# Performance work log

Measured on AMD Instinct MI355X. Metric: run time of the kernel, lower is better.

The kernel has to match this reference:

```python
import jax, jax.numpy as jnp
import numpy as np

DROPOUT_P = 0.0  # undefined global `dropout_p` in source; pinned to 0 (identity) for determinism


def setup_inputs() -> dict:
    key = jax.random.key(0)
    k1, k2, k3 = jax.random.split(key, 3)
    B, Lq, Lk, D = 16, 4096, 4096, 64
    return {
        "query": jax.random.normal(k1, (B, Lq, D), dtype=jnp.float32),
        "key": jax.random.normal(k2, (B, Lk, D), dtype=jnp.float32),
        "value": jax.random.normal(k3, (B, Lk, D), dtype=jnp.float32),
        "scale_factor": jnp.ones((1,), dtype=jnp.float32),
    }


def reference(query, key, value, scale_factor):
    # scores: [B, Lq, Lk] -- the large HBM-materialized intermediate
    scores = jnp.einsum("bqd,bkd->bqk", query, key) / scale_factor
    probs = jax.nn.softmax(scores, axis=-1)
    # dropout with p = DROPOUT_P = 0.0 is the identity
    out = jnp.einsum("bqk,bkd->bqd", probs, value)
    return out
```

## Files before the change

### kernel.cpp

```cpp
#include <hip/hip_runtime.h>
#include <hip/hip_fp16.h>

typedef _Float16 half2_t __attribute__((ext_vector_type(2)));
typedef _Float16 half4_t __attribute__((ext_vector_type(4)));
typedef _Float16 half8_t __attribute__((ext_vector_type(8)));
typedef float   float4_t __attribute__((ext_vector_type(4)));

static __device__ __forceinline__ half2_t cvt_pk(float a, float b) {
    return __builtin_bit_cast(half2_t, __builtin_amdgcn_cvt_pkrtz(a, b));
}
static __device__ __forceinline__ half4_t cvt_pk4(float a, float b, float c, float d) {
    half2_t lo = cvt_pk(a, b), hi = cvt_pk(c, d);
    half4_t r;
    r[0] = lo[0]; r[1] = lo[1]; r[2] = hi[0]; r[3] = hi[1];
    return r;
}

namespace {
constexpr int kB      = 16;
constexpr int kL      = 4096;
constexpr int kD      = 64;
constexpr int kQTile  = 128;
constexpr int kBK     = 64;
constexpr int kStride = 72;
}

__global__ __launch_bounds__(256, 2)
void fa_fwd(const float* __restrict__ Q, const float* __restrict__ K,
            const float* __restrict__ V, const float* __restrict__ scale_ptr,
            float* __restrict__ Out)
{
    __shared__ __align__(16) _Float16 Ksh[kBK * kStride];
    __shared__ __align__(16) _Float16 Vsh[kD * kStride];

    const int tid  = threadIdx.x;
    const int wave = tid >> 6;
    const int lane = tid & 63;
    const int c    = lane & 15;
    const int qd   = lane >> 4;

    const int b  = blockIdx.y;
    const int q0 = blockIdx.x * kQTile + wave * 32;

    const float qscale = 1.4426950408889634f / scale_ptr[0];

    const float* Qb = Q + (size_t)b * kL * kD;
    const float* Kb = K + (size_t)b * kL * kD;
    const float* Vb = V + (size_t)b * kL * kD;

    half8_t qfrag[2][2];
#pragma unroll
    for (int qt = 0; qt < 2; ++qt) {
        const float* qrow = Qb + (size_t)(q0 + qt * 16 + c) * kD;
#pragma unroll
        for (int dk = 0; dk < 2; ++dk) {
            const float* p = qrow + dk * 32 + qd * 8;
            half8_t h;
#pragma unroll
            for (int j = 0; j < 8; ++j) h[j] = (_Float16)(p[j] * qscale);
            qfrag[qt][dk] = h;
        }
    }

    float4_t O[2][4];
#pragma unroll
    for (int qt = 0; qt < 2; ++qt)
#pragma unroll
        for (int dt = 0; dt < 4; ++dt) O[qt][dt] = (float4_t)0.0f;

    float m_run[2] = {-__builtin_inff(), -__builtin_inff()};
    float lpart[2] = {0.0f, 0.0f};

    float4 pk[4], pv[4];
#pragma unroll
    for (int i = 0; i < 4; ++i) {
        const int tk = tid + 256 * i;
        pk[i] = *(const float4*)(Kb + (size_t)(tk >> 4) * kD + (tk & 15) * 4);
        pv[i] = *(const float4*)(Vb + (size_t)(tk & 63) * kD + (tk >> 6) * 4);
    }

    for (int kb = 0; kb < kL; kb += kBK) {
        __syncthreads();

#pragma unroll
        for (int i = 0; i < 4; ++i) {
            const int tk = tid + 256 * i;
            *(half4_t*)(&Ksh[(tk >> 4) * kStride + (tk & 15) * 4]) =
                cvt_pk4(pk[i].x, pk[i].y, pk[i].z, pk[i].w);
        }
#pragma unroll
        for (int i = 0; i < 4; ++i) {
            const int tk  = tid + 256 * i;
            const int row = tk & 63;
            const int c4  = tk >> 6;
            Vsh[(c4 * 4 + 0) * kStride + row] = (_Float16)pv[i].x;
            Vsh[(c4 * 4 + 1) * kStride + row] = (_Float16)pv[i].y;
            Vsh[(c4 * 4 + 2) * kStride + row] = (_Float16)pv[i].z;
            Vsh[(c4 * 4 + 3) * kStride + row] = (_Float16)pv[i].w;
        }
        __syncthreads();

        {
            const int nb = (kb + kBK) & (kL - 1);
            const float* Kn = Kb + (size_t)nb * kD;
            const float* Vn = Vb + (size_t)nb * kD;
#pragma unroll
            for (int i = 0; i < 4; ++i) {
                const int tk = tid + 256 * i;
                pk[i] = *(const float4*)(Kn + (size_t)(tk >> 4) * kD + (tk & 15) * 4);
                pv[i] = *(const float4*)(Vn + (size_t)(tk & 63) * kD + (tk >> 6) * 4);
            }
        }

        half8_t kf[4][2];
#pragma unroll
        for (int kt = 0; kt < 4; ++kt)
#pragma unroll
            for (int dk = 0; dk < 2; ++dk)
                kf[kt][dk] = *(const half8_t*)(&Ksh[(kt * 16 + c) * kStride + dk * 32 + qd * 8]);

        float4_t S[4][2];
#pragma unroll
        for (int kt = 0; kt < 4; ++kt)
#pragma unroll
            for (int qt = 0; qt < 2; ++qt) {
                float4_t acc = {-32.0f, -32.0f, -32.0f, -32.0f};
                acc = __builtin_amdgcn_mfma_f32_16x16x32_f16(kf[kt][0], qfrag[qt][0], acc, 0, 0, 0);
                acc = __builtin_amdgcn_mfma_f32_16x16x32_f16(kf[kt][1], qfrag[qt][1], acc, 0, 0, 0);
                S[kt][qt] = acc;
            }

        half4_t pf[4][2];
#pragma unroll
        for (int qt = 0; qt < 2; ++qt) {
            float tm = S[0][qt][0];
#pragma unroll
            for (int kt = 0; kt < 4; ++kt)
#pragma unroll
                for (int r = 0; r < 4; ++r) tm = fmaxf(tm, S[kt][qt][r]);
            tm = fmaxf(tm, __shfl_xor(tm, 16));
            tm = fmaxf(tm, __shfl_xor(tm, 32));

            const bool newmax = tm > m_run[qt];
            const float mn = newmax ? tm : m_run[qt];
            if (__ballot(newmax)) {
                const float alpha = __builtin_amdgcn_exp2f(m_run[qt] - mn);
                m_run[qt] = mn;
                lpart[qt] *= alpha;
#pragma unroll
                for (int r = 0; r < 4; ++r) {
                    const float a = __shfl(alpha, qd * 4 + r);
#pragma unroll
                    for (int dt = 0; dt < 4; ++dt) O[qt][dt][r] *= a;
                }
            }

#pragma unroll
            for (int kt = 0; kt < 4; ++kt) {
                const float p0 = __builtin_amdgcn_exp2f(S[kt][qt][0] - mn);
                const float p1 = __builtin_amdgcn_exp2f(S[kt][qt][1] - mn);
                const float p2 = __builtin_amdgcn_exp2f(S[kt][qt][2] - mn);
                const float p3 = __builtin_amdgcn_exp2f(S[kt][qt][3] - mn);
                lpart[qt] += (p0 + p1) + (p2 + p3);
                pf[kt][qt] = cvt_pk4(p0, p1, p2, p3);
            }
        }

#pragma unroll
        for (int kt = 0; kt < 4; ++kt)
#pragma unroll
            for (int dt = 0; dt < 4; ++dt) {
                const half4_t vf = *(const half4_t*)(&Vsh[(dt * 16 + c) * kStride + kt * 16 + qd * 4]);
#pragma unroll
                for (int qt = 0; qt < 2; ++qt)
                    O[qt][dt] = __builtin_amdgcn_mfma_f32_16x16x16f16(pf[kt][qt], vf, O[qt][dt], 0, 0, 0);
            }
    }

#pragma unroll
    for (int qt = 0; qt < 2; ++qt) {
        lpart[qt] += __shfl_xor(lpart[qt], 16);
        lpart[qt] += __shfl_xor(lpart[qt], 32);
    }

#pragma unroll
    for (int qt = 0; qt < 2; ++qt)
#pragma unroll
        for (int r = 0; r < 4; ++r) {
            const float lr  = __shfl(lpart[qt], qd * 4 + r);
            const float inv = 1.0f / lr;
            const int qrow  = q0 + qt * 16 + qd * 4 + r;
            float* op = Out + ((size_t)b * kL + qrow) * kD;
#pragma unroll
            for (int dt = 0; dt < 4; ++dt)
                op[dt * 16 + c] = O[qt][dt][r] * inv;
        }
}

extern "C" void kernel_launch(void* const* d_in, const int* in_sizes, int n_in,
                              void* d_out, int out_size, void* d_ws, size_t ws_size,
                              hipStream_t stream) {
    const float* Q = (const float*)d_in[0];
    const float* K = (const float*)d_in[1];
    const float* V = (const float*)d_in[2];
    const float* s = (const float*)d_in[3];
    float* out = (float*)d_out;
    dim3 grid(kL / kQTile, kB, 1);
    dim3 block(256, 1, 1);
    fa_fwd<<<grid, block, 0, stream>>>(Q, K, V, s, out);
}
```

Before: 214.3 us.

## Split key dimension across two blocks with workspace combine pass

Splits the key range of each attention block into two halves processed by separate blocks, writing unnormalized partial outputs plus running max and sum to a workspace. A second kernel merges the two partials with log-sum-exp weights. Launch bounds are raised to four blocks per CU to increase occupancy. This adds substantial extra global memory traffic and a second launch, and the tighter register budget risks spills.

```diff
diff --git a/kernel.cpp b/kernel.cpp
--- a/kernel.cpp
+++ b/kernel.cpp
@@ -23,12 +23,16 @@
 constexpr int kQTile  = 128;
 constexpr int kBK     = 64;
 constexpr int kStride = 72;
-}
-
-__global__ __launch_bounds__(256, 2)
+constexpr size_t kOS  = (size_t)kB * kL * kD;
+constexpr size_t kRS  = (size_t)kB * kL;
+constexpr size_t kWsFloats = 2 * kOS + 4 * kRS;
+}
+
+template <int SPLITS>
+__global__ __launch_bounds__(256, 4)
 void fa_fwd(const float* __restrict__ Q, const float* __restrict__ K,
             const float* __restrict__ V, const float* __restrict__ scale_ptr,
-            float* __restrict__ Out)
+            float* __restrict__ Out, float* __restrict__ ws)
 {
     __shared__ __align__(16) _Float16 Ksh[kBK * kStride];
     __shared__ __align__(16) _Float16 Vsh[kD * kStride];
@@ -39,8 +43,11 @@
     const int c    = lane & 15;
     const int qd   = lane >> 4;
 
-    const int b  = blockIdx.y;
-    const int q0 = blockIdx.x * kQTile + wave * 32;
+    const int b   = blockIdx.y;
+    const int z   = blockIdx.z;
+    const int q0  = blockIdx.x * kQTile + wave * 32;
+    const int ks0 = z * (kL / SPLITS);
+    const int ks1 = ks0 + kL / SPLITS;
 
     const float qscale = 1.4426950408889634f / scale_ptr[0];
 
@@ -75,11 +82,11 @@
 #pragma unroll
     for (int i = 0; i < 4; ++i) {
         const int tk = tid + 256 * i;
-        pk[i] = *(const float4*)(Kb + (size_t)(tk >> 4) * kD + (tk & 15) * 4);
-        pv[i] = *(const float4*)(Vb + (size_t)(tk & 63) * kD + (tk >> 6) * 4);
-    }
-
-    for (int kb = 0; kb < kL; kb += kBK) {
+        pk[i] = *(const float4*)(Kb + (size_t)(ks0 + (tk >> 4)) * kD + (tk & 15) * 4);
+        pv[i] = *(const float4*)(Vb + (size_t)(ks0 + (tk & 63)) * kD + (tk >> 6) * 4);
+    }
+
+    for (int kb = ks0; kb < ks1; kb += kBK) {
         __syncthreads();
 
 #pragma unroll
@@ -101,7 +108,7 @@
         __syncthreads();
 
         {
-            const int nb = (kb + kBK) & (kL - 1);
+            const int nb = (kb + kBK < ks1) ? kb + kBK : ks0;
             const float* Kn = Kb + (size_t)nb * kD;
             const float* Vn = Vb + (size_t)nb * kD;
 #pragma unroll
@@ -184,17 +191,61 @@
     }
 
 #pragma unroll
-    for (int qt = 0; qt < 2; ++qt)
-#pragma unroll
-        for (int r = 0; r < 4; ++r) {
-            const float lr  = __shfl(lpart[qt], qd * 4 + r);
-            const float inv = 1.0f / lr;
-            const int qrow  = q0 + qt * 16 + qd * 4 + r;
-            float* op = Out + ((size_t)b * kL + qrow) * kD;
-#pragma unroll
-            for (int dt = 0; dt < 4; ++dt)
-                op[dt * 16 + c] = O[qt][dt][r] * inv;
-        }
+    for (int qt = 0; qt < 2; ++qt) {
+        if (SPLITS == 1) {
+#pragma unroll
+            for (int r = 0; r < 4; ++r) {
+                const float lr  = __shfl(lpart[qt], qd * 4 + r);
+                const float inv = 1.0f / lr;
+                const int qrow  = q0 + qt * 16 + qd * 4 + r;
+                float* op = Out + ((size_t)b * kL + qrow) * kD;
+#pragma unroll
+                for (int dt = 0; dt < 4; ++dt)
+                    op[dt * 16 + c] = O[qt][dt][r] * inv;
+            }
+        } else {
+            float* Ow = ws + (size_t)z * kOS;
+#pragma unroll
+            for (int r = 0; r < 4; ++r) {
+                const int qrow = q0 + qt * 16 + qd * 4 + r;
+                float* op = Ow + ((size_t)b * kL + qrow) * kD;
+#pragma unroll
+                for (int dt = 0; dt < 4; ++dt)
+                    op[dt * 16 + c] = O[qt][dt][r];
+            }
+            if (qd == 0) {
+                const size_t row = (size_t)b * kL + q0 + qt * 16 + c;
+                ws[2 * kOS + (size_t)z * kRS + row]           = m_run[qt];
+                ws[2 * kOS + 2 * kRS + (size_t)z * kRS + row] = lpart[qt];
+            }
+        }
+    }
+}
+
+__global__ __launch_bounds__(256)
+void fa_combine(const float* __restrict__ ws, float* __restrict__ Out)
+{
+    const size_t j   = (size_t)blockIdx.x * 256 + threadIdx.x;
+    const size_t f   = j * 4;
+    const size_t row = f >> 6;
+
+    const float m0 = ws[2 * kOS + row];
+    const float m1 = ws[2 * kOS + kRS + row];
+    const float l0 = ws[2 * kOS + 2 * kRS + row];
+    const float l1 = ws[2 * kOS + 3 * kRS + row];
+    const float M  = fmaxf(m0, m1);
+    const float w0 = __builtin_amdgcn_exp2f(m0 - M);
+    const float w1 = __builtin_amdgcn_exp2f(m1 - M);
+    const float inv = 1.0f / (l0 * w0 + l1 * w1);
+
+    const float4 a = *(const float4*)(ws + f);
+    const float4 bq = *(const float4*)(ws + kOS + f);
+    float4 o;
+    o.x = (a.x * w0 + bq.x * w1) * inv;
+    o.y = (a.y * w0 + bq.y * w1) * inv;
+    o.z = (a.z * w0 + bq.z * w1) * inv;
+    o.w = (a.w * w0 + bq.w * w1) * inv;
+    *(float4*)(Out + f) = o;
 }
 
 extern "C" void kernel_launch(void* const* d_in, const int* in_sizes, int n_in,
@@ -205,7 +256,14 @@
     const float* V = (const float*)d_in[2];
     const float* s = (const float*)d_in[3];
     float* out = (float*)d_out;
-    dim3 grid(kL / kQTile, kB, 1);
-    dim3 block(256, 1, 1);
-    fa_fwd<<<grid, block, 0, stream>>>(Q, K, V, s, out);
-}
+    float* ws  = (float*)d_ws;
+
+    if (ws_size >= kWsFloats * sizeof(float)) {
+        dim3 grid(kL / kQTile, kB, 2);
+        fa_fwd<2><<<grid, dim3(256, 1, 1), 0, stream>>>(Q, K, V, s, out, ws);
+        fa_combine<<<dim3((unsigned)(kOS / (256 * 4))), dim3(256, 1, 1), 0, stream>>>(ws, out);
+    } else {
+        dim3 grid(kL / kQTile, kB, 1);
+        fa_fwd<1><<<grid, dim3(256, 1, 1), 0, stream>>>(Q, K, V, s, out, ws);
+    }
+}
```

After: 459.9 us. +114.7%, slower.

## Split key range across two wave groups per block and merge partial softmax

Applied to the files above, without the earlier changes.

Doubles the block to 512 threads and splits them into two 4-wave groups. Each group processes half of the key/value sequence for the same 128 queries, using its own shared-memory K/V tiles. At the end, group 1 writes its partial O, running max and row sum to shared memory, and group 0 combines them with log-sum-exp rescaling before writing the output. The aim is to double the resident waves per CU and so hide latency better. The stricter launch bound (512 threads, 4 blocks) can cap registers low enough to cause spills.

```diff
diff --git a/kernel.cpp b/kernel.cpp
--- a/kernel.cpp
+++ b/kernel.cpp
@@ -23,24 +23,33 @@
 constexpr int kQTile  = 128;
 constexpr int kBK     = 64;
 constexpr int kStride = 72;
-}
-
-__global__ __launch_bounds__(256, 2)
+constexpr int kTileHalfs = kBK * kStride;
+constexpr int kGrpHalfs  = 2 * kTileHalfs;
+}
+
+__global__ __launch_bounds__(512, 4)
 void fa_fwd(const float* __restrict__ Q, const float* __restrict__ K,
             const float* __restrict__ V, const float* __restrict__ scale_ptr,
             float* __restrict__ Out)
 {
-    __shared__ __align__(16) _Float16 Ksh[kBK * kStride];
-    __shared__ __align__(16) _Float16 Vsh[kD * kStride];
+    __shared__ __align__(16) char smem[2 * kGrpHalfs * sizeof(_Float16)];
 
     const int tid  = threadIdx.x;
     const int wave = tid >> 6;
+    const int g    = wave >> 2;
+    const int w4   = wave & 3;
+    const int tg   = tid & 255;
     const int lane = tid & 63;
     const int c    = lane & 15;
     const int qd   = lane >> 4;
 
-    const int b  = blockIdx.y;
-    const int q0 = blockIdx.x * kQTile + wave * 32;
+    _Float16* Ksh = (_Float16*)smem + g * kGrpHalfs;
+    _Float16* Vsh = Ksh + kTileHalfs;
+
+    const int b   = blockIdx.y;
+    const int q0  = blockIdx.x * kQTile + w4 * 32;
+    const int ks0 = g * (kL / 2);
+    const int ks1 = ks0 + kL / 2;
 
     const float qscale = 1.4426950408889634f / scale_ptr[0];
 
@@ -74,23 +83,23 @@
     float4 pk[4], pv[4];
 #pragma unroll
     for (int i = 0; i < 4; ++i) {
-        const int tk = tid + 256 * i;
-        pk[i] = *(const float4*)(Kb + (size_t)(tk >> 4) * kD + (tk & 15) * 4);
-        pv[i] = *(const float4*)(Vb + (size_t)(tk & 63) * kD + (tk >> 6) * 4);
-    }
-
-    for (int kb = 0; kb < kL; kb += kBK) {
+        const int tk = tg + 256 * i;
+        pk[i] = *(const float4*)(Kb + (size_t)(ks0 + (tk >> 4)) * kD + (tk & 15) * 4);
+        pv[i] = *(const float4*)(Vb + (size_t)(ks0 + (tk & 63)) * kD + (tk >> 6) * 4);
+    }
+
+    for (int kb = ks0; kb < ks1; kb += kBK) {
         __syncthreads();
 
 #pragma unroll
         for (int i = 0; i < 4; ++i) {
-            const int tk = tid + 256 * i;
+            const int tk = tg + 256 * i;
             *(half4_t*)(&Ksh[(tk >> 4) * kStride + (tk & 15) * 4]) =
                 cvt_pk4(pk[i].x, pk[i].y, pk[i].z, pk[i].w);
         }
 #pragma unroll
         for (int i = 0; i < 4; ++i) {
-            const int tk  = tid + 256 * i;
+            const int tk  = tg + 256 * i;
             const int row = tk & 63;
             const int c4  = tk >> 6;
             Vsh[(c4 * 4 + 0) * kStride + row] = (_Float16)pv[i].x;
@@ -101,12 +110,12 @@
         __syncthreads();
 
         {
-            const int nb = (kb + kBK) & (kL - 1);
+            const int nb = (kb + kBK < ks1) ? kb + kBK : ks0;
             const float* Kn = Kb + (size_t)nb * kD;
             const float* Vn = Vb + (size_t)nb * kD;
 #pragma unroll
             for (int i = 0; i < 4; ++i) {
-                const int tk = tid + 256 * i;
+                const int tk = tg + 256 * i;
                 pk[i] = *(const float4*)(Kn + (size_t)(tk >> 4) * kD + (tk & 15) * 4);
                 pv[i] = *(const float4*)(Vn + (size_t)(tk & 63) * kD + (tk >> 6) * 4);
             }
@@ -183,18 +192,52 @@
         lpart[qt] += __shfl_xor(lpart[qt], 32);
     }
 
-#pragma unroll
-    for (int qt = 0; qt < 2; ++qt)
-#pragma unroll
-        for (int r = 0; r < 4; ++r) {
-            const float lr  = __shfl(lpart[qt], qd * 4 + r);
-            const float inv = 1.0f / lr;
-            const int qrow  = q0 + qt * 16 + qd * 4 + r;
-            float* op = Out + ((size_t)b * kL + qrow) * kD;
-#pragma unroll
-            for (int dt = 0; dt < 4; ++dt)
-                op[dt * 16 + c] = O[qt][dt][r] * inv;
-        }
+    __syncthreads();
+
+    float* Osh = (float*)smem;
+    float* Msh = Osh + 4 * 32 * 64;
+    float* Lsh = Msh + 128;
+
+    if (g == 1) {
+#pragma unroll
+        for (int qt = 0; qt < 2; ++qt) {
+#pragma unroll
+            for (int r = 0; r < 4; ++r) {
+                const int row = qt * 16 + qd * 4 + r;
+                float* op = Osh + w4 * 2048 + row * 64;
+#pragma unroll
+                for (int dt = 0; dt < 4; ++dt)
+                    op[dt * 16 + c] = O[qt][dt][r];
+            }
+            if (qd == 0) {
+                Msh[(w4 * 2 + qt) * 16 + c] = m_run[qt];
+                Lsh[(w4 * 2 + qt) * 16 + c] = lpart[qt];
+            }
+        }
+    }
+    __syncthreads();
+
+    if (g == 0) {
+#pragma unroll
+        for (int qt = 0; qt < 2; ++qt)
+#pragma unroll
+            for (int r = 0; r < 4; ++r) {
+                const int row   = qt * 16 + qd * 4 + r;
+                const float m0r = __shfl(m_run[qt], qd * 4 + r);
+                const float l0r = __shfl(lpart[qt], qd * 4 + r);
+                const float m1r = Msh[(w4 * 2 + qt) * 16 + qd * 4 + r];
+                const float l1r = Lsh[(w4 * 2 + qt) * 16 + qd * 4 + r];
+                const float M   = fmaxf(m0r, m1r);
+                const float w0  = __builtin_amdgcn_exp2f(m0r - M);
+                const float w1  = __builtin_amdgcn_exp2f(m1r - M);
+                const float inv = 1.0f / (l0r * w0 + l1r * w1);
+                const float* osrc = Osh + w4 * 2048 + row * 64;
+                float* op = Out + ((size_t)b * kL + q0 + row) * kD;
+#pragma unroll
+                for (int dt = 0; dt < 4; ++dt)
+                    op[dt * 16 + c] = (O[qt][dt][r] * w0 + osrc[dt * 16 + c] * w1) * inv;
+            }
+    }
 }
 
 extern "C" void kernel_launch(void* const* d_in, const int* in_sizes, int n_in,
@@ -206,6 +249,6 @@
     const float* s = (const float*)d_in[3];
     float* out = (float*)d_out;
     dim3 grid(kL / kQTile, kB, 1);
-    dim3 block(256, 1, 1);
+    dim3 block(512, 1, 1);
     fa_fwd<<<grid, block, 0, stream>>>(Q, K, V, s, out);
 }
```

New measurement: 530.5 us. 148% more time.
